# Kernel optimization log

Hardware: AMD Instinct MI355X
Metric: run time of the kernel (lower is better)

Reference implementation:

```python
import jax, jax.numpy as jnp
import numpy as np


def setup_inputs() -> dict:
    key = jax.random.key(0)
    ks = jax.random.split(key, 6)
    b, l, d, n = 4, 2048, 1024, 16
    scale_d = 1.0 / np.sqrt(d)
    x = jax.random.normal(ks[0], (b, l, d), dtype=jnp.float32)
    W1 = jax.random.normal(ks[1], (d, d), dtype=jnp.float32) * scale_d
    b1 = jnp.zeros((d,), dtype=jnp.float32)
    W2 = jax.random.normal(ks[2], (n, d), dtype=jnp.float32) * scale_d
    b2 = jnp.zeros((n,), dtype=jnp.float32)
    W3 = jax.random.normal(ks[3], (n, d), dtype=jnp.float32) * scale_d
    b3 = jnp.zeros((n,), dtype=jnp.float32)
    A = jax.random.normal(ks[4], (d, n), dtype=jnp.float32) * np.sqrt(2.0 / (d + n))
    return {"x": x, "W1": W1, "b1": b1, "W2": W2, "b2": b2, "W3": W3, "b3": b3, "A": A}


def reference(x, W1, b1, W2, b2, W3, b3, A):
    # delta = softplus(fc1(x)); B = fc2(x); C = fc3(x)
    delta = jax.nn.softplus(jnp.einsum('bld,ed->ble', x, W1) + b1)   # (b,l,d)
    B = jnp.einsum('bld,nd->bln', x, W2) + b2                         # (b,l,n)
    C = jnp.einsum('bld,nd->bln', x, W3) + b3                         # (b,l,n)
    # Discretization: dB = delta \otimes B; dA = exp(delta \otimes A).
    # In the original forward, h is zero-initialized so dA * h == 0 exactly
    # (for both values and gradients); h_new = x[...,None] * dB.
    dB = jnp.einsum('bld,bln->bldn', delta, B)                        # (b,l,d,n)
    h = x[..., None] * dB                                             # (b,l,d,n)
    y = jnp.einsum('bln,bldn->bld', C, h)                             # (b,l,d)
    return y
```

## Files before the change

### kernel.cpp

```cpp
#include <hip/hip_runtime.h>
#include <hip/hip_bf16.h>

typedef __attribute__((ext_vector_type(8))) short bf16x8;
typedef __attribute__((ext_vector_type(8))) unsigned short u16x8;
typedef __attribute__((ext_vector_type(4))) unsigned short u16x4;
typedef __attribute__((ext_vector_type(4))) float f32x4;

#define DDIM 1024
#define BM 256
#define BN 128
#define BK 64

__device__ __forceinline__ void gload_lds16(const void* g, void* l) {
  __builtin_amdgcn_global_load_lds((const __attribute__((address_space(1))) void*)g,
                                   (__attribute__((address_space(3))) void*)l,
                                   16, 0, 0);
}

__device__ __forceinline__ unsigned short f2bf(float f) {
  unsigned int u = __float_as_uint(f);
  unsigned int r = (u + 0x7FFFu + ((u >> 16) & 1u)) >> 16;
  return (unsigned short)r;
}

__global__ __launch_bounds__(256) void s6_convert(
    const float* __restrict__ X, const float* __restrict__ W1,
    const float* __restrict__ W2, const float* __restrict__ W3,
    unsigned short* __restrict__ Xbf, unsigned short* __restrict__ W1bf,
    unsigned short* __restrict__ W2bf, unsigned short* __restrict__ W3bf)
{
  const int i   = blockIdx.x * 256 + threadIdx.x;
  const int row = i >> 8;
  const int off = (i & 255) * 4;

  const float* src;
  unsigned short* dst;
  if (row < 8192)      { src = X  + (size_t)row * DDIM;        dst = Xbf  + (size_t)row * DDIM; }
  else if (row < 9216) { int r = row - 8192; src = W1 + (size_t)r * DDIM; dst = W1bf + (size_t)r * DDIM; }
  else if (row < 9232) { int r = row - 9216; src = W2 + (size_t)r * DDIM; dst = W2bf + (size_t)r * DDIM; }
  else                 { int r = row - 9232; src = W3 + (size_t)r * DDIM; dst = W3bf + (size_t)r * DDIM; }

  const float4 v = *reinterpret_cast<const float4*>(src + off);
  u16x4 o;
  o[0] = f2bf(v.x); o[1] = f2bf(v.y); o[2] = f2bf(v.z); o[3] = f2bf(v.w);
  *reinterpret_cast<u16x4*>(dst + off) = o;
}

__global__ __launch_bounds__(512, 2) void s6_main_fused(
    const unsigned short* __restrict__ Xbf,
    const unsigned short* __restrict__ W1bf,
    const unsigned short* __restrict__ W2bf,
    const unsigned short* __restrict__ W3bf,
    const float* __restrict__ b1,
    const float* __restrict__ b2,
    const float* __restrict__ b3,
    float* __restrict__ Y)
{
  __shared__ __align__(16) unsigned short lds[2 * 16384 + 2 * 12288];
  unsigned short* AB = lds;
  unsigned short* BB = lds + 2 * 16384;

  const int tid  = threadIdx.x;
  const int wid  = tid >> 6;
  const int lane = tid & 63;
  const int tile = (blockIdx.x & 7) * 32 + (blockIdx.x >> 3);
  const int rb   = tile >> 3;
  const int cb   = tile & 7;
  const int row0 = rb * BM;
  const int col0 = cb * BN;
  const int wr = wid >> 1, wc = wid & 1;

  const f32x4 z4 = {0.f, 0.f, 0.f, 0.f};
  f32x4 acc[4][4];
  #pragma unroll
  for (int i = 0; i < 4; ++i)
    #pragma unroll
    for (int j = 0; j < 4; ++j)
      acc[i][j] = z4;
  f32x4 accS[4] = {z4, z4, z4, z4};

  const int srow = tid >> 3;
  const int sdch = (lane & 7) ^ (lane >> 3);
  const unsigned short* gaBase = Xbf  + (size_t)(row0 + srow) * DDIM + sdch * 8;
  const unsigned short* gbBase = W1bf + (size_t)(col0 + srow) * DDIM + sdch * 8;
  const int sub = srow;
  const unsigned short* gwsrc;
  if (sub < 16)      gwsrc = W2bf + (size_t)sub * DDIM;
  else if (sub < 32) gwsrc = W3bf + (size_t)(sub - 16) * DDIM;
  else               gwsrc = W2bf + (size_t)(sub & 15) * DDIM;
  const unsigned short* gwBase = gwsrc + sdch * 8;

  const int fr = lane & 15;
  const int swz0 = (((lane >> 4) + 0) ^ (fr & 7)) * 8;
  const int swz1 = (((lane >> 4) + 4) ^ (fr & 7)) * 8;

#define STAGE(BUF, KEL) do {                                                   \
    const unsigned short* sa_ = gaBase + (KEL);                                \
    const unsigned short* sb_ = gbBase + (KEL);                                \
    unsigned short* la_ = AB + (BUF) * 16384 + wid * 512;                      \
    unsigned short* lb_ = BB + (BUF) * 12288 + wid * 512;                      \
    gload_lds16(sa_,                la_);                                      \
    gload_lds16(sa_ +  64 * DDIM,   la_ + 4096);                               \
    gload_lds16(sa_ + 128 * DDIM,   la_ + 8192);                               \
    gload_lds16(sa_ + 192 * DDIM,   la_ + 12288);                              \
    gload_lds16(sb_,                lb_);                                      \
    gload_lds16(sb_ +  64 * DDIM,   lb_ + 4096);                               \
    gload_lds16(gwBase + (KEL),     lb_ + 8192);                               \
  } while (0)

#define COMPUTE(PAR) do {                                                      \
    const unsigned short* Al = AB + (PAR) * 16384;                             \
    const unsigned short* Bl = BB + (PAR) * 12288;                             \
    bf16x8 af[4][2], bfr[4][2], wfr[2];                                        \
    _Pragma("unroll")                                                          \
    for (int m = 0; m < 4; ++m) {                                              \
      af[m][0] = *reinterpret_cast<const bf16x8*>(&Al[(wr*64 + m*16 + fr)*BK + swz0]); \
      af[m][1] = *reinterpret_cast<const bf16x8*>(&Al[(wr*64 + m*16 + fr)*BK + swz1]); \
    }                                                                          \
    _Pragma("unroll")                                                          \
    for (int n = 0; n < 4; ++n) {                                              \
      bfr[n][0] = *reinterpret_cast<const bf16x8*>(&Bl[(wc*64 + n*16 + fr)*BK + swz0]); \
      bfr[n][1] = *reinterpret_cast<const bf16x8*>(&Bl[(wc*64 + n*16 + fr)*BK + swz1]); \
    }                                                                          \
    wfr[0] = *reinterpret_cast<const bf16x8*>(&Bl[(128 + wc*16 + fr)*BK + swz0]); \
    wfr[1] = *reinterpret_cast<const bf16x8*>(&Bl[(128 + wc*16 + fr)*BK + swz1]); \
    __builtin_amdgcn_s_setprio(1);                                             \
    _Pragma("unroll")                                                          \
    for (int ks = 0; ks < 2; ++ks) {                                           \
      _Pragma("unroll")                                                        \
      for (int m = 0; m < 4; ++m) {                                            \
        _Pragma("unroll")                                                      \
        for (int n = 0; n < 4; ++n)                                            \
          acc[m][n] = __builtin_amdgcn_mfma_f32_16x16x32_bf16(af[m][ks], bfr[n][ks], acc[m][n], 0, 0, 0); \
        accS[m] = __builtin_amdgcn_mfma_f32_16x16x32_bf16(af[m][ks], wfr[ks], accS[m], 0, 0, 0); \
      }                                                                        \
    }                                                                          \
    __builtin_amdgcn_s_setprio(0);                                             \
  } while (0)

#define STEP(J, PAR) do {                                                      \
    if ((J) < 15) {                                                            \
      STAGE((PAR) ^ 1, ((J) + 1) * BK);                                        \
      asm volatile("s_waitcnt vmcnt(7)" ::: "memory");                         \
    } else {                                                                   \
      asm volatile("s_waitcnt vmcnt(0)" ::: "memory");                         \
    }                                                                          \
    __builtin_amdgcn_s_barrier();                                              \
    __builtin_amdgcn_sched_barrier(0);                                         \
    COMPUTE(PAR);                                                              \
    __builtin_amdgcn_s_barrier();                                              \
  } while (0)

  STAGE(0, 0);
  asm volatile("s_waitcnt vmcnt(0)" ::: "memory");
  __builtin_amdgcn_s_barrier();

  for (int jj = 0; jj < 16; jj += 2) {
    STEP(jj, 0);
    STEP(jj + 1, 1);
  }
#undef STEP
#undef COMPUTE
#undef STAGE

  float* sEx = (float*)lds;
  const int n_  = lane & 15;
  const int rgp = (lane >> 4) * 4;
  const float bSelf = (wc == 0 ? b2[n_] : b3[n_]);
  #pragma unroll
  for (int m = 0; m < 4; ++m)
    #pragma unroll
    for (int q = 0; q < 4; ++q)
      sEx[(wc * 256 + wr * 64 + m * 16 + rgp + q) * 17 + n_] = accS[m][q] + bSelf;
  __syncthreads();

  float sv[4][4];
  #pragma unroll
  for (int m = 0; m < 4; ++m) {
    #pragma unroll
    for (int q = 0; q < 4; ++q) {
      const float other = sEx[((wc ^ 1) * 256 + wr * 64 + m * 16 + rgp + q) * 17 + n_];
      float p = (accS[m][q] + bSelf) * other;
      p += __shfl_xor(p, 1, 64);
      p += __shfl_xor(p, 2, 64);
      p += __shfl_xor(p, 4, 64);
      p += __shfl_xor(p, 8, 64);
      sv[m][q] = p;
    }
  }

  #pragma unroll
  for (int m = 0; m < 4; ++m) {
    #pragma unroll
    for (int q = 0; q < 4; ++q) {
      const int gr = row0 + wr * 64 + m * 16 + rgp + q;
      const float svv = sv[m][q];
      const size_t rbase = (size_t)gr * DDIM;
      #pragma unroll
      for (int n = 0; n < 4; ++n) {
        const int gc = col0 + wc * 64 + n * 16 + fr;
        const float z  = acc[m][n][q] + b1[gc];
        const float e  = exp2f(-1.44269504f * fabsf(z));
        const float sp = fmaxf(z, 0.f) + 0.69314718f * log2f(1.f + e);
        const float xv = __bfloat162float(*(const __hip_bfloat16*)&Xbf[rbase + gc]);
        Y[rbase + gc] = xv * svv * sp;
      }
    }
  }
}

extern "C" void kernel_launch(void* const* d_in, const int* in_sizes, int n_in,
                              void* d_out, int out_size, void* d_ws, size_t ws_size,
                              hipStream_t stream) {
  const float* x  = (const float*)d_in[0];
  const float* W1 = (const float*)d_in[1];
  const float* b1 = (const float*)d_in[2];
  const float* W2 = (const float*)d_in[3];
  const float* b2 = (const float*)d_in[4];
  const float* W3 = (const float*)d_in[5];
  const float* b3 = (const float*)d_in[6];

  char* ws = (char*)d_ws;
  unsigned short* Xbf  = (unsigned short*)(ws);
  unsigned short* W1bf = (unsigned short*)(ws + 16777216);
  unsigned short* W2bf = (unsigned short*)(ws + 16777216 + 2097152);
  unsigned short* W3bf = (unsigned short*)(ws + 16777216 + 2097152 + 32768);

  s6_convert<<<9248, 256, 0, stream>>>(x, W1, W2, W3, Xbf, W1bf, W2bf, W3bf);
  s6_main_fused<<<256, 512, 0, stream>>>(Xbf, W1bf, W2bf, W3bf, b1, b2, b3,
                                         (float*)d_out);
}
```

Before: 44.65 us.

## Halve GEMM row tile to 128 and launch 512 blocks with higher occupancy

Cuts the block row tile from 256 to 128, so 512 blocks are launched instead of 256. This spreads the work over all 256 CUs with two blocks each, and the launch bound now allows four blocks per CU. LDS per block shrinks and each wave holds half as many accumulators. Per k-step fragment loads are interleaved with the MFMAs to lower register pressure. The trade-off is that W1 and the W2/W3 slice are re-read for twice as many row tiles, and each staged load feeds fewer MFMAs, so arithmetic intensity drops.

```diff
diff --git a/kernel.cpp b/kernel.cpp
--- a/kernel.cpp
+++ b/kernel.cpp
@@ -7,7 +7,7 @@
 typedef __attribute__((ext_vector_type(4))) float f32x4;
 
 #define DDIM 1024
-#define BM 256
+#define BM 128
 #define BN 128
 #define BK 64
 
@@ -46,7 +46,7 @@
   *reinterpret_cast<u16x4*>(dst + off) = o;
 }
 
-__global__ __launch_bounds__(512, 2) void s6_main_fused(
+__global__ __launch_bounds__(512, 4) void s6_main_fused(
     const unsigned short* __restrict__ Xbf,
     const unsigned short* __restrict__ W1bf,
     const unsigned short* __restrict__ W2bf,
@@ -56,14 +56,14 @@
     const float* __restrict__ b3,
     float* __restrict__ Y)
 {
-  __shared__ __align__(16) unsigned short lds[2 * 16384 + 2 * 12288];
+  __shared__ __align__(16) unsigned short lds[2 * 8192 + 2 * 12288];
   unsigned short* AB = lds;
-  unsigned short* BB = lds + 2 * 16384;
+  unsigned short* BB = lds + 2 * 8192;
 
   const int tid  = threadIdx.x;
   const int wid  = tid >> 6;
   const int lane = tid & 63;
-  const int tile = (blockIdx.x & 7) * 32 + (blockIdx.x >> 3);
+  const int tile = (blockIdx.x & 7) * 64 + (blockIdx.x >> 3);
   const int rb   = tile >> 3;
   const int cb   = tile & 7;
   const int row0 = rb * BM;
@@ -71,13 +71,13 @@
   const int wr = wid >> 1, wc = wid & 1;
 
   const f32x4 z4 = {0.f, 0.f, 0.f, 0.f};
-  f32x4 acc[4][4];
-  #pragma unroll
-  for (int i = 0; i < 4; ++i)
+  f32x4 acc[2][4];
+  #pragma unroll
+  for (int i = 0; i < 2; ++i)
     #pragma unroll
     for (int j = 0; j < 4; ++j)
       acc[i][j] = z4;
-  f32x4 accS[4] = {z4, z4, z4, z4};
+  f32x4 accS[2] = {z4, z4};
 
   const int srow = tid >> 3;
   const int sdch = (lane & 7) ^ (lane >> 3);
@@ -97,51 +97,47 @@
 #define STAGE(BUF, KEL) do {                                                   \
     const unsigned short* sa_ = gaBase + (KEL);                                \
     const unsigned short* sb_ = gbBase + (KEL);                                \
-    unsigned short* la_ = AB + (BUF) * 16384 + wid * 512;                      \
+    unsigned short* la_ = AB + (BUF) * 8192  + wid * 512;                      \
     unsigned short* lb_ = BB + (BUF) * 12288 + wid * 512;                      \
-    gload_lds16(sa_,                la_);                                      \
-    gload_lds16(sa_ +  64 * DDIM,   la_ + 4096);                               \
-    gload_lds16(sa_ + 128 * DDIM,   la_ + 8192);                               \
-    gload_lds16(sa_ + 192 * DDIM,   la_ + 12288);                              \
-    gload_lds16(sb_,                lb_);                                      \
-    gload_lds16(sb_ +  64 * DDIM,   lb_ + 4096);                               \
-    gload_lds16(gwBase + (KEL),     lb_ + 8192);                               \
+    gload_lds16(sa_,              la_);                                        \
+    gload_lds16(sa_ + 64 * DDIM,  la_ + 4096);                                 \
+    gload_lds16(sb_,              lb_);                                        \
+    gload_lds16(sb_ + 64 * DDIM,  lb_ + 4096);                                 \
+    gload_lds16(gwBase + (KEL),   lb_ + 8192);                                 \
   } while (0)
 
 #define COMPUTE(PAR) do {                                                      \
-    const unsigned short* Al = AB + (PAR) * 16384;                             \
+    const unsigned short* Al = AB + (PAR) * 8192;                              \
     const unsigned short* Bl = BB + (PAR) * 12288;                             \
-    bf16x8 af[4][2], bfr[4][2], wfr[2];                                        \
-    _Pragma("unroll")                                                          \
-    for (int m = 0; m < 4; ++m) {                                              \
-      af[m][0] = *reinterpret_cast<const bf16x8*>(&Al[(wr*64 + m*16 + fr)*BK + swz0]); \
-      af[m][1] = *reinterpret_cast<const bf16x8*>(&Al[(wr*64 + m*16 + fr)*BK + swz1]); \
-    }                                                                          \
-    _Pragma("unroll")                                                          \
-    for (int n = 0; n < 4; ++n) {                                              \
-      bfr[n][0] = *reinterpret_cast<const bf16x8*>(&Bl[(wc*64 + n*16 + fr)*BK + swz0]); \
-      bfr[n][1] = *reinterpret_cast<const bf16x8*>(&Bl[(wc*64 + n*16 + fr)*BK + swz1]); \
-    }                                                                          \
-    wfr[0] = *reinterpret_cast<const bf16x8*>(&Bl[(128 + wc*16 + fr)*BK + swz0]); \
-    wfr[1] = *reinterpret_cast<const bf16x8*>(&Bl[(128 + wc*16 + fr)*BK + swz1]); \
-    __builtin_amdgcn_s_setprio(1);                                             \
     _Pragma("unroll")                                                          \
     for (int ks = 0; ks < 2; ++ks) {                                           \
-      _Pragma("unroll")                                                        \
-      for (int m = 0; m < 4; ++m) {                                            \
-        _Pragma("unroll")                                                      \
-        for (int n = 0; n < 4; ++n)                                            \
-          acc[m][n] = __builtin_amdgcn_mfma_f32_16x16x32_bf16(af[m][ks], bfr[n][ks], acc[m][n], 0, 0, 0); \
-        accS[m] = __builtin_amdgcn_mfma_f32_16x16x32_bf16(af[m][ks], wfr[ks], accS[m], 0, 0, 0); \
-      }                                                                        \
+      const int swz = ks ? swz1 : swz0;                                        \
+      bf16x8 a0 = *reinterpret_cast<const bf16x8*>(&Al[(wr*32 +  0 + fr)*BK + swz]); \
+      bf16x8 a1 = *reinterpret_cast<const bf16x8*>(&Al[(wr*32 + 16 + fr)*BK + swz]); \
+      bf16x8 g0 = *reinterpret_cast<const bf16x8*>(&Bl[(wc*64 +  0 + fr)*BK + swz]); \
+      bf16x8 g1 = *reinterpret_cast<const bf16x8*>(&Bl[(wc*64 + 16 + fr)*BK + swz]); \
+      bf16x8 g2 = *reinterpret_cast<const bf16x8*>(&Bl[(wc*64 + 32 + fr)*BK + swz]); \
+      bf16x8 g3 = *reinterpret_cast<const bf16x8*>(&Bl[(wc*64 + 48 + fr)*BK + swz]); \
+      bf16x8 wf = *reinterpret_cast<const bf16x8*>(&Bl[(128 + wc*16 + fr)*BK + swz]); \
+      __builtin_amdgcn_s_setprio(1);                                           \
+      acc[0][0] = __builtin_amdgcn_mfma_f32_16x16x32_bf16(a0, g0, acc[0][0], 0, 0, 0); \
+      acc[0][1] = __builtin_amdgcn_mfma_f32_16x16x32_bf16(a0, g1, acc[0][1], 0, 0, 0); \
+      acc[0][2] = __builtin_amdgcn_mfma_f32_16x16x32_bf16(a0, g2, acc[0][2], 0, 0, 0); \
+      acc[0][3] = __builtin_amdgcn_mfma_f32_16x16x32_bf16(a0, g3, acc[0][3], 0, 0, 0); \
+      acc[1][0] = __builtin_amdgcn_mfma_f32_16x16x32_bf16(a1, g0, acc[1][0], 0, 0, 0); \
+      acc[1][1] = __builtin_amdgcn_mfma_f32_16x16x32_bf16(a1, g1, acc[1][1], 0, 0, 0); \
+      acc[1][2] = __builtin_amdgcn_mfma_f32_16x16x32_bf16(a1, g2, acc[1][2], 0, 0, 0); \
+      acc[1][3] = __builtin_amdgcn_mfma_f32_16x16x32_bf16(a1, g3, acc[1][3], 0, 0, 0); \
+      accS[0]   = __builtin_amdgcn_mfma_f32_16x16x32_bf16(a0, wf, accS[0], 0, 0, 0); \
+      accS[1]   = __builtin_amdgcn_mfma_f32_16x16x32_bf16(a1, wf, accS[1], 0, 0, 0); \
+      __builtin_amdgcn_s_setprio(0);                                           \
     }                                                                          \
-    __builtin_amdgcn_s_setprio(0);                                             \
   } while (0)
 
 #define STEP(J, PAR) do {                                                      \
     if ((J) < 15) {                                                            \
       STAGE((PAR) ^ 1, ((J) + 1) * BK);                                        \
-      asm volatile("s_waitcnt vmcnt(7)" ::: "memory");                         \
+      asm volatile("s_waitcnt vmcnt(5)" ::: "memory");                         \
     } else {                                                                   \
       asm volatile("s_waitcnt vmcnt(0)" ::: "memory");                         \
     }                                                                          \
@@ -168,18 +164,18 @@
   const int rgp = (lane >> 4) * 4;
   const float bSelf = (wc == 0 ? b2[n_] : b3[n_]);
   #pragma unroll
-  for (int m = 0; m < 4; ++m)
+  for (int m = 0; m < 2; ++m)
     #pragma unroll
     for (int q = 0; q < 4; ++q)
-      sEx[(wc * 256 + wr * 64 + m * 16 + rgp + q) * 17 + n_] = accS[m][q] + bSelf;
+      sEx[(wc * 128 + wr * 32 + m * 16 + rgp + q) * 17 + n_] = accS[m][q] + bSelf;
   __syncthreads();
 
-  float sv[4][4];
-  #pragma unroll
-  for (int m = 0; m < 4; ++m) {
+  float sv[2][4];
+  #pragma unroll
+  for (int m = 0; m < 2; ++m) {
     #pragma unroll
     for (int q = 0; q < 4; ++q) {
-      const float other = sEx[((wc ^ 1) * 256 + wr * 64 + m * 16 + rgp + q) * 17 + n_];
+      const float other = sEx[((wc ^ 1) * 128 + wr * 32 + m * 16 + rgp + q) * 17 + n_];
       float p = (accS[m][q] + bSelf) * other;
       p += __shfl_xor(p, 1, 64);
       p += __shfl_xor(p, 2, 64);
@@ -190,10 +186,10 @@
   }
 
   #pragma unroll
-  for (int m = 0; m < 4; ++m) {
+  for (int m = 0; m < 2; ++m) {
     #pragma unroll
     for (int q = 0; q < 4; ++q) {
-      const int gr = row0 + wr * 64 + m * 16 + rgp + q;
+      const int gr = row0 + wr * 32 + m * 16 + rgp + q;
       const float svv = sv[m][q];
       const size_t rbase = (size_t)gr * DDIM;
       #pragma unroll
@@ -227,6 +223,6 @@
   unsigned short* W3bf = (unsigned short*)(ws + 16777216 + 2097152 + 32768);
 
   s6_convert<<<9248, 256, 0, stream>>>(x, W1, W2, W3, Xbf, W1bf, W2bf, W3bf);
-  s6_main_fused<<<256, 512, 0, stream>>>(Xbf, W1bf, W2bf, W3bf, b1, b2, b3,
+  s6_main_fused<<<512, 512, 0, stream>>>(Xbf, W1bf, W2bf, W3bf, b1, b2, b3,
                                          (float*)d_out);
 }
```

After: 43.61 us. 2.3% less time.
